# Kernel optimization log

Measured on AMD Instinct MI355X. Metric: run time of the kernel, lower is better.

## Reference

```python
import jax, jax.numpy as jnp
import numpy as np

DROPOUT_P = 0.0  # undefined global `dropout_p` in source; pinned to 0 (identity) for determinism


def setup_inputs() -> dict:
    key = jax.random.key(0)
    k1, k2, k3 = jax.random.split(key, 3)
    B, Lq, Lk, D = 16, 4096, 4096, 64
    return {
        "query": jax.random.normal(k1, (B, Lq, D), dtype=jnp.float32),
        "key": jax.random.normal(k2, (B, Lk, D), dtype=jnp.float32),
        "value": jax.random.normal(k3, (B, Lk, D), dtype=jnp.float32),
        "scale_factor": jnp.ones((1,), dtype=jnp.float32),
    }


def reference(query, key, value, scale_factor):
    # scores: [B, Lq, Lk] -- the large HBM-materialized intermediate
    scores = jnp.einsum("bqd,bkd->bqk", query, key) / scale_factor
    probs = jax.nn.softmax(scores, axis=-1)
    # dropout with p = DROPOUT_P = 0.0 is the identity
    out = jnp.einsum("bqk,bkd->bqd", probs, value)
    return out
```

## Files before the change

### kernel.cpp

```cpp
#include <hip/hip_runtime.h>
#include <hip/hip_fp16.h>

typedef _Float16 half2_t __attribute__((ext_vector_type(2)));
typedef _Float16 half4_t __attribute__((ext_vector_type(4)));
typedef _Float16 half8_t __attribute__((ext_vector_type(8)));
typedef float   float4_t __attribute__((ext_vector_type(4)));

static __device__ __forceinline__ half2_t cvt_pk(float a, float b) {
    return __builtin_bit_cast(half2_t, __builtin_amdgcn_cvt_pkrtz(a, b));
}
static __device__ __forceinline__ half4_t cvt_pk4(float a, float b, float c, float d) {
    half2_t lo = cvt_pk(a, b), hi = cvt_pk(c, d);
    half4_t r;
    r[0] = lo[0]; r[1] = lo[1]; r[2] = hi[0]; r[3] = hi[1];
    return r;
}

namespace {
constexpr int kB       = 16;
constexpr int kL       = 4096;
constexpr int kD       = 64;
constexpr int kQTile   = 128;
constexpr int kBK      = 64;
constexpr int kKStride = 72;
constexpr int kVStride = 68;
}

__global__ __launch_bounds__(256, 2)
void fa_fwd(const float* __restrict__ Q, const float* __restrict__ K,
            const float* __restrict__ V, const float* __restrict__ scale_ptr,
            float* __restrict__ Out)
{
    __shared__ __align__(16) _Float16 Ksh[kBK * kKStride];
    __shared__ __align__(16) _Float16 Vsh[kD * kVStride];

    const int tid  = threadIdx.x;
    const int wave = tid >> 6;
    const int lane = tid & 63;
    const int c    = lane & 15;
    const int qd   = lane >> 4;

    const int b  = blockIdx.y;
    const int q0 = blockIdx.x * kQTile + wave * 32;

    const int vd = tid & 63;
    const int vk = tid >> 6;

    const float qscale = 1.4426950408889634f / scale_ptr[0];

    const float* Qb = Q + (size_t)b * kL * kD;
    const float* Kb = K + (size_t)b * kL * kD;
    const float* Vb = V + (size_t)b * kL * kD;

    half8_t qfrag[2][2];
#pragma unroll
    for (int qt = 0; qt < 2; ++qt) {
        const float* qrow = Qb + (size_t)(q0 + qt * 16 + c) * kD;
#pragma unroll
        for (int dk = 0; dk < 2; ++dk) {
            const float* p = qrow + dk * 32 + qd * 8;
            half8_t h;
#pragma unroll
            for (int j = 0; j < 8; ++j) h[j] = (_Float16)(p[j] * qscale);
            qfrag[qt][dk] = h;
        }
    }

    float4_t O[2][4];
#pragma unroll
    for (int qt = 0; qt < 2; ++qt)
#pragma unroll
        for (int dt = 0; dt < 4; ++dt) O[qt][dt] = (float4_t)0.0f;

    float m_run[2] = {-__builtin_inff(), -__builtin_inff()};
    float lpart[2] = {0.0f, 0.0f};

    float4 pka[2], pkb[2];
    float pv[16];
#pragma unroll
    for (int i2 = 0; i2 < 2; ++i2) {
        const int tk = tid + 256 * i2;
        const float* src = Kb + (size_t)(tk >> 3) * kD + (tk & 7) * 8;
        pka[i2] = *(const float4*)(src);
        pkb[i2] = *(const float4*)(src + 4);
    }
#pragma unroll
    for (int i = 0; i < 4; ++i)
#pragma unroll
        for (int j = 0; j < 4; ++j)
            pv[i * 4 + j] = Vb[(size_t)(i * 16 + vk * 4 + j) * kD + vd];

    for (int kb = 0; kb < kL; kb += kBK) {
        __syncthreads();

#pragma unroll
        for (int i2 = 0; i2 < 2; ++i2) {
            const int tk = tid + 256 * i2;
            half4_t lo = cvt_pk4(pka[i2].x, pka[i2].y, pka[i2].z, pka[i2].w);
            half4_t hi = cvt_pk4(pkb[i2].x, pkb[i2].y, pkb[i2].z, pkb[i2].w);
            half8_t h8 = __builtin_shufflevector(lo, hi, 0, 1, 2, 3, 4, 5, 6, 7);
            *(half8_t*)(&Ksh[(tk >> 3) * kKStride + (tk & 7) * 8]) = h8;
        }
#pragma unroll
        for (int i = 0; i < 4; ++i) {
            *(half4_t*)(&Vsh[vd * kVStride + i * 16 + vk * 4]) =
                cvt_pk4(pv[i * 4 + 0], pv[i * 4 + 1], pv[i * 4 + 2], pv[i * 4 + 3]);
        }
        __syncthreads();

        {
            const int nb = (kb + kBK < kL) ? kb + kBK : 0;
            const float* Kn = Kb + (size_t)nb * kD;
            const float* Vn = Vb + (size_t)nb * kD;
#pragma unroll
            for (int i2 = 0; i2 < 2; ++i2) {
                const int tk = tid + 256 * i2;
                const float* src = Kn + (size_t)(tk >> 3) * kD + (tk & 7) * 8;
                pka[i2] = *(const float4*)(src);
                pkb[i2] = *(const float4*)(src + 4);
            }
#pragma unroll
            for (int i = 0; i < 4; ++i)
#pragma unroll
                for (int j = 0; j < 4; ++j)
                    pv[i * 4 + j] = Vn[(size_t)(i * 16 + vk * 4 + j) * kD + vd];
        }

        half8_t kf[4][2];
#pragma unroll
        for (int kt = 0; kt < 4; ++kt)
#pragma unroll
            for (int dk = 0; dk < 2; ++dk)
                kf[kt][dk] = *(const half8_t*)(&Ksh[(kt * 16 + c) * kKStride + dk * 32 + qd * 8]);

        float4_t S[4][2];
#pragma unroll
        for (int kt = 0; kt < 4; ++kt)
#pragma unroll
            for (int qt = 0; qt < 2; ++qt) {
                float4_t acc = {-32.0f, -32.0f, -32.0f, -32.0f};
                acc = __builtin_amdgcn_mfma_f32_16x16x32_f16(kf[kt][0], qfrag[qt][0], acc, 0, 0, 0);
                acc = __builtin_amdgcn_mfma_f32_16x16x32_f16(kf[kt][1], qfrag[qt][1], acc, 0, 0, 0);
                S[kt][qt] = acc;
            }

        half4_t pf[4][2];
#pragma unroll
        for (int qt = 0; qt < 2; ++qt) {
            float tm = S[0][qt][0];
#pragma unroll
            for (int kt = 0; kt < 4; ++kt)
#pragma unroll
                for (int r = 0; r < 4; ++r) tm = fmaxf(tm, S[kt][qt][r]);
            tm = fmaxf(tm, __shfl_xor(tm, 16));
            tm = fmaxf(tm, __shfl_xor(tm, 32));

            const bool newmax = tm > m_run[qt];
            const float mn = newmax ? tm : m_run[qt];
            if (__ballot(newmax)) {
                const float alpha = __builtin_amdgcn_exp2f(m_run[qt] - mn);
                m_run[qt] = mn;
                lpart[qt] *= alpha;
#pragma unroll
                for (int r = 0; r < 4; ++r) {
                    const float a = __shfl(alpha, qd * 4 + r);
#pragma unroll
                    for (int dt = 0; dt < 4; ++dt) O[qt][dt][r] *= a;
                }
            }

#pragma unroll
            for (int kt = 0; kt < 4; ++kt) {
                const float p0 = __builtin_amdgcn_exp2f(S[kt][qt][0] - mn);
                const float p1 = __builtin_amdgcn_exp2f(S[kt][qt][1] - mn);
                const float p2 = __builtin_amdgcn_exp2f(S[kt][qt][2] - mn);
                const float p3 = __builtin_amdgcn_exp2f(S[kt][qt][3] - mn);
                lpart[qt] += (p0 + p1) + (p2 + p3);
                pf[kt][qt] = cvt_pk4(p0, p1, p2, p3);
            }
        }

#pragma unroll
        for (int kt = 0; kt < 4; ++kt)
#pragma unroll
            for (int dt = 0; dt < 4; ++dt) {
                const half4_t vf = *(const half4_t*)(&Vsh[(dt * 16 + c) * kVStride + kt * 16 + qd * 4]);
#pragma unroll
                for (int qt = 0; qt < 2; ++qt)
                    O[qt][dt] = __builtin_amdgcn_mfma_f32_16x16x16f16(pf[kt][qt], vf, O[qt][dt], 0, 0, 0);
            }
    }

#pragma unroll
    for (int qt = 0; qt < 2; ++qt) {
        lpart[qt] += __shfl_xor(lpart[qt], 16);
        lpart[qt] += __shfl_xor(lpart[qt], 32);
    }

#pragma unroll
    for (int qt = 0; qt < 2; ++qt)
#pragma unroll
        for (int r = 0; r < 4; ++r) {
            const float lr  = __shfl(lpart[qt], qd * 4 + r);
            const float inv = 1.0f / lr;
            const int qrow  = q0 + qt * 16 + qd * 4 + r;
            float* op = Out + ((size_t)b * kL + qrow) * kD;
#pragma unroll
            for (int dt = 0; dt < 4; ++dt)
                op[dt * 16 + c] = O[qt][dt][r] * inv;
        }
}

extern "C" void kernel_launch(void* const* d_in, const int* in_sizes, int n_in,
                              void* d_out, int out_size, void* d_ws, size_t ws_size,
                              hipStream_t stream) {
    const float* Q = (const float*)d_in[0];
    const float* K = (const float*)d_in[1];
    const float* V = (const float*)d_in[2];
    const float* s = (const float*)d_in[3];
    float* out = (float*)d_out;
    dim3 grid(kL / kQTile, kB, 1);
    dim3 block(256, 1, 1);
    fa_fwd<<<grid, block, 0, stream>>>(Q, K, V, s, out);
}
```

Baseline: 204.9 us.

## Pre-convert K/V to fp16 tiles in workspace and compute row sums via MFMA

```diff
diff --git a/kernel.cpp b/kernel.cpp
--- a/kernel.cpp
+++ b/kernel.cpp
@@ -14,6 +14,11 @@
     half4_t r;
     r[0] = lo[0]; r[1] = lo[1]; r[2] = hi[0]; r[3] = hi[1];
     return r;
+}
+static __device__ __forceinline__ half8_t cvt_pk8(const float4& a, const float4& b) {
+    half4_t lo = cvt_pk4(a.x, a.y, a.z, a.w);
+    half4_t hi = cvt_pk4(b.x, b.y, b.z, b.w);
+    return __builtin_shufflevector(lo, hi, 0, 1, 2, 3, 4, 5, 6, 7);
 }
 
 namespace {
@@ -22,13 +27,56 @@
 constexpr int kD       = 64;
 constexpr int kQTile   = 128;
 constexpr int kBK      = 64;
+constexpr int kTiles   = kL / kBK;
+constexpr int kTileH   = kBK * kD;
 constexpr int kKStride = 72;
 constexpr int kVStride = 68;
+constexpr size_t kWsHalves = (size_t)kB * kTiles * kTileH;
+}
+
+
+__global__ __launch_bounds__(256) void prep_kv(const float* __restrict__ K,
+                                               const float* __restrict__ V,
+                                               _Float16* __restrict__ Kws,
+                                               _Float16* __restrict__ Vws)
+{
+    int blk = blockIdx.x;
+    const int tid = threadIdx.x;
+    if (blk < kB * kTiles) {
+        const float* src = K + (size_t)blk * kTileH;
+        _Float16* dst = Kws + (size_t)blk * kTileH;
+#pragma unroll
+        for (int i = 0; i < 2; ++i) {
+            const int task = tid + 256 * i;
+            const float* p = src + task * 8;
+            const float4 a  = *(const float4*)p;
+            const float4 b2 = *(const float4*)(p + 4);
+            *(half8_t*)(dst + task * 8) = cvt_pk8(a, b2);
+        }
+    } else {
+        blk -= kB * kTiles;
+        const float* src = V + (size_t)blk * kTileH;
+        _Float16* dst = Vws + (size_t)blk * kTileH;
+        const int d  = tid & 63;
+        const int vw = tid >> 6;
+#pragma unroll
+        for (int i = 0; i < 2; ++i) {
+            const int c8 = vw * 2 + i;
+            const int k0 = c8 * 8;
+            float p[8];
+#pragma unroll
+            for (int j = 0; j < 8; ++j) p[j] = src[(k0 + j) * kD + d];
+            half4_t lo = cvt_pk4(p[0], p[1], p[2], p[3]);
+            half4_t hi = cvt_pk4(p[4], p[5], p[6], p[7]);
+            *(half8_t*)(dst + (c8 * 64 + d) * 8) =
+                __builtin_shufflevector(lo, hi, 0, 1, 2, 3, 4, 5, 6, 7);
+        }
+    }
 }
 
 __global__ __launch_bounds__(256, 2)
-void fa_fwd(const float* __restrict__ Q, const float* __restrict__ K,
-            const float* __restrict__ V, const float* __restrict__ scale_ptr,
+void fa_fwd(const float* __restrict__ Q, const _Float16* __restrict__ Kws,
+            const _Float16* __restrict__ Vws, const float* __restrict__ scale_ptr,
             float* __restrict__ Out)
 {
     __shared__ __align__(16) _Float16 Ksh[kBK * kKStride];
@@ -43,14 +91,15 @@
     const int b  = blockIdx.y;
     const int q0 = blockIdx.x * kQTile + wave * 32;
 
+    const int task0 = tid, task1 = tid + 256;
     const int vd = tid & 63;
-    const int vk = tid >> 6;
+    const int vw = tid >> 6;
 
     const float qscale = 1.4426950408889634f / scale_ptr[0];
 
-    const float* Qb = Q + (size_t)b * kL * kD;
-    const float* Kb = K + (size_t)b * kL * kD;
-    const float* Vb = V + (size_t)b * kL * kD;
+    const float*    Qb = Q   + (size_t)b * kL * kD;
+    const _Float16* Kt = Kws + (size_t)b * kTiles * kTileH;
+    const _Float16* Vt = Vws + (size_t)b * kTiles * kTileH;
 
     half8_t qfrag[2][2];
 #pragma unroll
@@ -67,63 +116,46 @@
     }
 
     float4_t O[2][4];
-#pragma unroll
-    for (int qt = 0; qt < 2; ++qt)
+    float4_t O5[2];
+#pragma unroll
+    for (int qt = 0; qt < 2; ++qt) {
+        O5[qt] = (float4_t)0.0f;
 #pragma unroll
         for (int dt = 0; dt < 4; ++dt) O[qt][dt] = (float4_t)0.0f;
-
+    }
     float m_run[2] = {-__builtin_inff(), -__builtin_inff()};
-    float lpart[2] = {0.0f, 0.0f};
-
-    float4 pka[2], pkb[2];
-    float pv[16];
-#pragma unroll
-    for (int i2 = 0; i2 < 2; ++i2) {
-        const int tk = tid + 256 * i2;
-        const float* src = Kb + (size_t)(tk >> 3) * kD + (tk & 7) * 8;
-        pka[i2] = *(const float4*)(src);
-        pkb[i2] = *(const float4*)(src + 4);
-    }
-#pragma unroll
-    for (int i = 0; i < 4; ++i)
-#pragma unroll
-        for (int j = 0; j < 4; ++j)
-            pv[i * 4 + j] = Vb[(size_t)(i * 16 + vk * 4 + j) * kD + vd];
-
-    for (int kb = 0; kb < kL; kb += kBK) {
+
+    const half4_t vone = {(_Float16)1.0f, (_Float16)1.0f, (_Float16)1.0f, (_Float16)1.0f};
+
+    half8_t kp[2], vp[2];
+    kp[0] = *(const half8_t*)(Kt + task0 * 8);
+    kp[1] = *(const half8_t*)(Kt + task1 * 8);
+    vp[0] = *(const half8_t*)(Vt + ((vw * 2 + 0) * 64 + vd) * 8);
+    vp[1] = *(const half8_t*)(Vt + ((vw * 2 + 1) * 64 + vd) * 8);
+
+    for (int t = 0; t < kTiles; ++t) {
         __syncthreads();
 
-#pragma unroll
-        for (int i2 = 0; i2 < 2; ++i2) {
-            const int tk = tid + 256 * i2;
-            half4_t lo = cvt_pk4(pka[i2].x, pka[i2].y, pka[i2].z, pka[i2].w);
-            half4_t hi = cvt_pk4(pkb[i2].x, pkb[i2].y, pkb[i2].z, pkb[i2].w);
-            half8_t h8 = __builtin_shufflevector(lo, hi, 0, 1, 2, 3, 4, 5, 6, 7);
-            *(half8_t*)(&Ksh[(tk >> 3) * kKStride + (tk & 7) * 8]) = h8;
-        }
-#pragma unroll
-        for (int i = 0; i < 4; ++i) {
-            *(half4_t*)(&Vsh[vd * kVStride + i * 16 + vk * 4]) =
-                cvt_pk4(pv[i * 4 + 0], pv[i * 4 + 1], pv[i * 4 + 2], pv[i * 4 + 3]);
+        *(half8_t*)(&Ksh[(task0 >> 3) * kKStride + (task0 & 7) * 8]) = kp[0];
+        *(half8_t*)(&Ksh[(task1 >> 3) * kKStride + (task1 & 7) * 8]) = kp[1];
+#pragma unroll
+        for (int i = 0; i < 2; ++i) {
+            const int c8 = vw * 2 + i;
+            *(half4_t*)(&Vsh[vd * kVStride + c8 * 8])     =
+                __builtin_shufflevector(vp[i], vp[i], 0, 1, 2, 3);
+            *(half4_t*)(&Vsh[vd * kVStride + c8 * 8 + 4]) =
+                __builtin_shufflevector(vp[i], vp[i], 4, 5, 6, 7);
         }
         __syncthreads();
 
         {
-            const int nb = (kb + kBK < kL) ? kb + kBK : 0;
-            const float* Kn = Kb + (size_t)nb * kD;
-            const float* Vn = Vb + (size_t)nb * kD;
-#pragma unroll
-            for (int i2 = 0; i2 < 2; ++i2) {
-                const int tk = tid + 256 * i2;
-                const float* src = Kn + (size_t)(tk >> 3) * kD + (tk & 7) * 8;
-                pka[i2] = *(const float4*)(src);
-                pkb[i2] = *(const float4*)(src + 4);
-            }
-#pragma unroll
-            for (int i = 0; i < 4; ++i)
-#pragma unroll
-                for (int j = 0; j < 4; ++j)
-                    pv[i * 4 + j] = Vn[(size_t)(i * 16 + vk * 4 + j) * kD + vd];
+            const int nt = (t + 1) & (kTiles - 1);
+            const _Float16* kn = Kt + (size_t)nt * kTileH;
+            const _Float16* vn = Vt + (size_t)nt * kTileH;
+            kp[0] = *(const half8_t*)(kn + task0 * 8);
+            kp[1] = *(const half8_t*)(kn + task1 * 8);
+            vp[0] = *(const half8_t*)(vn + ((vw * 2 + 0) * 64 + vd) * 8);
+            vp[1] = *(const half8_t*)(vn + ((vw * 2 + 1) * 64 + vd) * 8);
         }
 
         half8_t kf[4][2];
@@ -160,12 +192,12 @@
             if (__ballot(newmax)) {
                 const float alpha = __builtin_amdgcn_exp2f(m_run[qt] - mn);
                 m_run[qt] = mn;
-                lpart[qt] *= alpha;
 #pragma unroll
                 for (int r = 0; r < 4; ++r) {
                     const float a = __shfl(alpha, qd * 4 + r);
 #pragma unroll
                     for (int dt = 0; dt < 4; ++dt) O[qt][dt][r] *= a;
+                    O5[qt][r] *= a;
                 }
             }
 
@@ -175,34 +207,31 @@
                 const float p1 = __builtin_amdgcn_exp2f(S[kt][qt][1] - mn);
                 const float p2 = __builtin_amdgcn_exp2f(S[kt][qt][2] - mn);
                 const float p3 = __builtin_amdgcn_exp2f(S[kt][qt][3] - mn);
-                lpart[qt] += (p0 + p1) + (p2 + p3);
                 pf[kt][qt] = cvt_pk4(p0, p1, p2, p3);
             }
         }
 
 #pragma unroll
-        for (int kt = 0; kt < 4; ++kt)
+        for (int kt = 0; kt < 4; ++kt) {
 #pragma unroll
             for (int dt = 0; dt < 4; ++dt) {
-                const half4_t vf = *(const half4_t*)(&Vsh[(dt * 16 + c) * kVStride + kt * 16 + qd * 4]);
+                const half4_t vf = *(const half4_t*)(
+                    &Vsh[(dt * 16 + c) * kVStride + kt * 16 + qd * 4]);
 #pragma unroll
                 for (int qt = 0; qt < 2; ++qt)
                     O[qt][dt] = __builtin_amdgcn_mfma_f32_16x16x16f16(pf[kt][qt], vf, O[qt][dt], 0, 0, 0);
             }
-    }
-
-#pragma unroll
-    for (int qt = 0; qt < 2; ++qt) {
-        lpart[qt] += __shfl_xor(lpart[qt], 16);
-        lpart[qt] += __shfl_xor(lpart[qt], 32);
+#pragma unroll
+            for (int qt = 0; qt < 2; ++qt)
+                O5[qt] = __builtin_amdgcn_mfma_f32_16x16x16f16(pf[kt][qt], vone, O5[qt], 0, 0, 0);
+        }
     }
 
 #pragma unroll
     for (int qt = 0; qt < 2; ++qt)
 #pragma unroll
         for (int r = 0; r < 4; ++r) {
-            const float lr  = __shfl(lpart[qt], qd * 4 + r);
-            const float inv = 1.0f / lr;
+            const float inv = 1.0f / O5[qt][r];
             const int qrow  = q0 + qt * 16 + qd * 4 + r;
             float* op = Out + ((size_t)b * kL + qrow) * kD;
 #pragma unroll
@@ -219,7 +248,9 @@
     const float* V = (const float*)d_in[2];
     const float* s = (const float*)d_in[3];
     float* out = (float*)d_out;
-    dim3 grid(kL / kQTile, kB, 1);
-    dim3 block(256, 1, 1);
-    fa_fwd<<<grid, block, 0, stream>>>(Q, K, V, s, out);
-}
+    _Float16* Kws = (_Float16*)d_ws;
+    _Float16* Vws = Kws + kWsHalves;
+
+    prep_kv<<<dim3(2 * kB * kTiles), dim3(256), 0, stream>>>(K, V, Kws, Vws);
+    fa_fwd<<<dim3(kL / kQTile, kB, 1), dim3(256), 0, stream>>>(Q, Kws, Vws, s, out);
+}
```

Result: faster. 200.4 us (-2.2%).
